# Performance work log

Hardware: AMD Instinct MI355X
Metric: run time of the kernel (lower is better)

Reference implementation:

```python
import jax, jax.numpy as jnp
import numpy as np


def setup_inputs() -> dict:
    key = jax.random.key(0)
    ks = jax.random.split(key, 4)
    B, Tq, Tv, D = 8, 256, 512, 256  # decoder_dim = D = 256
    query = jax.random.normal(ks[0], (B, Tq, D), dtype=jnp.float32)
    value = jax.random.normal(ks[1], (B, Tv, D), dtype=jnp.float32)
    W1 = jax.random.normal(ks[2], (D, D), dtype=jnp.float32) * (1.0 / np.sqrt(D))
    b1 = jnp.zeros((D,), dtype=jnp.float32)
    W2 = jax.random.normal(ks[3], (D, D), dtype=jnp.float32) * (1.0 / np.sqrt(D))
    b2 = jnp.zeros((D,), dtype=jnp.float32)
    return {"query": query, "value": value, "W1": W1, "b1": b1, "W2": W2, "b2": b2}


def reference(query, value, W1, b1, W2, b2):
    # Dense projections: [B,Tq,D], [B,Tv,D]
    q = jnp.einsum('bqd,de->bqe', query, W1) + b1
    v = jnp.einsum('bvd,de->bve', value, W2) + b2
    # Additive (Bahdanau) score: broadcast tanh then reduce over feature dim
    # score: [B,Tq,Tv]  (intermediate [B,Tq,Tv,D] is the fusion target)
    score = jnp.tanh(q[:, :, None, :] + v[:, None, :, :]).sum(axis=-1)
    alignment = jax.nn.softmax(score, axis=-1)  # [B,Tq,Tv]
    context = jnp.einsum('bqv,bvd->bqd', alignment, value)  # [B,Tq,D]
    context = jnp.concatenate([context, query], axis=-1)  # [B,Tq,2D]
    alignment_t = jnp.transpose(alignment, (0, 2, 1))  # [B,Tv,Tq]
    return context, alignment_t
```

## Files before the change

kernel.cpp:

```cpp
#include <hip/hip_runtime.h>

#define B_  8
#define TQ  256
#define TV  512
#define DD  256
#define ALGS 520

__device__ __forceinline__ float fast_exp2(float x) {
#if __has_builtin(__builtin_amdgcn_exp2f)
  return __builtin_amdgcn_exp2f(x);
#else
  return __exp2f(x);
#endif
}
__device__ __forceinline__ float fast_rcp(float x) {
#if __has_builtin(__builtin_amdgcn_rcpf)
  return __builtin_amdgcn_rcpf(x);
#else
  return 1.0f / x;
#endif
}

__global__ __launch_bounds__(256) void proj_fused(
    const float* __restrict__ query, const float* __restrict__ value,
    const float* __restrict__ W1, const float* __restrict__ b1,
    const float* __restrict__ W2, const float* __restrict__ b2,
    float* __restrict__ qp, float* __restrict__ vp, float scale) {
  __shared__ float As[2][32][64];
  __shared__ float Bs[2][32][64];
  const int t  = threadIdx.x;
  const int rt = blockIdx.x;
  const int bn = blockIdx.y << 6;

  const float* A; const float* W; const float* bias; float* out; int row0;
  if (rt < 32) { row0 = rt << 6;        A = query; W = W1; bias = b1; out = qp; }
  else         { row0 = (rt - 32) << 6; A = value; W = W2; bias = b2; out = vp; }

  const int tx = t & 15, ty = t >> 4;
  const int aar = t >> 3, aac = (t & 7) << 2;
  const int bbr = t >> 4, bbc = (t & 15) << 2;

  float4 ra[2], rb[2];
#pragma unroll
  for (int it = 0; it < 2; ++it) {
    ra[it] = *(const float4*)(A + (size_t)(row0 + (it << 5) + aar) * DD + aac);
    rb[it] = *(const float4*)(W + (size_t)((it << 4) + bbr) * DD + bn + bbc);
  }
#pragma unroll
  for (int it = 0; it < 2; ++it) {
    const int m = (it << 5) + aar;
#pragma unroll
    for (int c = 0; c < 4; ++c) {
      const int k = aac + c;
      As[0][k][m ^ (((k >> 2) & 7) << 2)] = (&ra[it].x)[c];
    }
    *(float4*)&Bs[0][(it << 4) + bbr][bbc] = rb[it];
  }
  __syncthreads();

  float acc[4][4] = {{0.f,0.f,0.f,0.f},{0.f,0.f,0.f,0.f},
                     {0.f,0.f,0.f,0.f},{0.f,0.f,0.f,0.f}};
  int p = 0;

  for (int k0 = 0; k0 < 256; k0 += 32) {
    const bool more = (k0 + 32) < 256;
    if (more) {
#pragma unroll
      for (int it = 0; it < 2; ++it) {
        ra[it] = *(const float4*)(A + (size_t)(row0 + (it << 5) + aar) * DD + k0 + 32 + aac);
        rb[it] = *(const float4*)(W + (size_t)(k0 + 32 + (it << 4) + bbr) * DD + bn + bbc);
      }
    }
#pragma unroll
    for (int k = 0; k < 32; ++k) {
      float4 aq = *(const float4*)&As[p][k][(ty << 2) ^ (((k >> 2) & 7) << 2)];
      float4 bq = *(const float4*)&Bs[p][k][tx << 2];
      acc[0][0] = fmaf(aq.x, bq.x, acc[0][0]); acc[0][1] = fmaf(aq.x, bq.y, acc[0][1]);
      acc[0][2] = fmaf(aq.x, bq.z, acc[0][2]); acc[0][3] = fmaf(aq.x, bq.w, acc[0][3]);
      acc[1][0] = fmaf(aq.y, bq.x, acc[1][0]); acc[1][1] = fmaf(aq.y, bq.y, acc[1][1]);
      acc[1][2] = fmaf(aq.y, bq.z, acc[1][2]); acc[1][3] = fmaf(aq.y, bq.w, acc[1][3]);
      acc[2][0] = fmaf(aq.z, bq.x, acc[2][0]); acc[2][1] = fmaf(aq.z, bq.y, acc[2][1]);
      acc[2][2] = fmaf(aq.z, bq.z, acc[2][2]); acc[2][3] = fmaf(aq.z, bq.w, acc[2][3]);
      acc[3][0] = fmaf(aq.w, bq.x, acc[3][0]); acc[3][1] = fmaf(aq.w, bq.y, acc[3][1]);
      acc[3][2] = fmaf(aq.w, bq.z, acc[3][2]); acc[3][3] = fmaf(aq.w, bq.w, acc[3][3]);
    }
    if (more) {
      const int q = p ^ 1;
#pragma unroll
      for (int it = 0; it < 2; ++it) {
        const int m = (it << 5) + aar;
#pragma unroll
        for (int c = 0; c < 4; ++c) {
          const int k = aac + c;
          As[q][k][m ^ (((k >> 2) & 7) << 2)] = (&ra[it].x)[c];
        }
        *(float4*)&Bs[q][(it << 4) + bbr][bbc] = rb[it];
      }
      __syncthreads();
      p = q;
    }
  }

  float4 bvv = *(const float4*)&bias[bn + (tx << 2)];
#pragma unroll
  for (int r = 0; r < 4; ++r) {
    float4 o;
    o.x = fast_exp2(scale * (acc[r][0] + bvv.x));
    o.y = fast_exp2(scale * (acc[r][1] + bvv.y));
    o.z = fast_exp2(scale * (acc[r][2] + bvv.z));
    o.w = fast_exp2(scale * (acc[r][3] + bvv.w));
    *(float4*)(out + (size_t)(row0 + (ty << 2) + r) * DD + bn + (tx << 2)) = o;
  }
}

__global__ __launch_bounds__(512, 4) void attn_kernel(
    const float* __restrict__ qp, const float* __restrict__ vp,
    const float* __restrict__ value, const float* __restrict__ query,
    float* __restrict__ out1, float* __restrict__ out2) {
  __shared__ float qs[4 * 256];
  __shared__ float alg[4 * ALGS];

  const int t    = threadIdx.x;
  const int lane = t & 63;
  const int wv   = t >> 6;
  const int jj   = lane >> 2;
  const int dq   = lane & 3;
  const int bb   = blockIdx.x & 7;
  const int i0   = (blockIdx.x >> 3) << 2;

  const float* vpb = vp + (size_t)bb * TV * DD;
  const float* qb  = qp + (size_t)(bb * TQ + i0) * DD;

  if (t < 256) {
    const int qi = t >> 6, qc = (t & 63) << 2;
    *(float4*)&qs[qi * 256 + qc] = *(const float4*)(qb + (size_t)qi * DD + qc);
  }
  __syncthreads();

  const int jb = (wv << 4) + jj;
  const float* vr0 = vpb + (size_t)jb * DD + (dq << 2);
  const float* vr1 = vr0 + 128 * DD;
  const float* vr2 = vr0 + 256 * DD;
  const float* vr3 = vr0 + 384 * DD;
  const float* qlane = qs + (dq << 2);

  float acc[4][4] = {{0.f,0.f,0.f,0.f},{0.f,0.f,0.f,0.f},
                     {0.f,0.f,0.f,0.f},{0.f,0.f,0.f,0.f}};

#pragma unroll 2
  for (int k = 0; k < 16; ++k) {
    const int doff = k << 4;
    float4 q0 = *(const float4*)(qlane + 0 * 256 + doff);
    float4 q1 = *(const float4*)(qlane + 1 * 256 + doff);
    float4 q2 = *(const float4*)(qlane + 2 * 256 + doff);
    float4 q3 = *(const float4*)(qlane + 3 * 256 + doff);
#pragma unroll
    for (int jg = 0; jg < 4; ++jg) {
      const float* vrp = (jg == 0) ? vr0 : (jg == 1) ? vr1 : (jg == 2) ? vr2 : vr3;
      float4 v4 = *(const float4*)(vrp + doff);
#pragma unroll
      for (int i = 0; i < 4; ++i) {
        const float4 q4 = (i == 0) ? q0 : (i == 1) ? q1 : (i == 2) ? q2 : q3;
        float a = q4.x * v4.x, b = q4.y * v4.y;
        float c = q4.z * v4.z, d = q4.w * v4.w;
        float sab = a + b,  scd = c + d;
        float Q1 = fmaf(a, b, sab + 1.f);
        float Q2 = fmaf(c, d, scd + 1.f);
        float N  = fmaf(scd + 2.f, Q1, (sab + 2.f) * Q2);
        acc[i][jg] = fmaf(N, fast_rcp(Q1 * Q2), acc[i][jg]);
      }
    }
  }

#pragma unroll
  for (int i = 0; i < 4; ++i)
#pragma unroll
    for (int jg = 0; jg < 4; ++jg) {
      acc[i][jg] += __shfl_xor(acc[i][jg], 1, 64);
      acc[i][jg] += __shfl_xor(acc[i][jg], 2, 64);
    }
#pragma unroll
  for (int jg = 0; jg < 4; ++jg) {
    float x = (dq == 0) ? acc[0][jg] : (dq == 1) ? acc[1][jg]
            : (dq == 2) ? acc[2][jg] : acc[3][jg];
    alg[dq * ALGS + (jg << 7) + jb] = x;
  }
  __syncthreads();

  if (wv < 4) {
    float s[8];
#pragma unroll
    for (int c = 0; c < 8; ++c) s[c] = alg[wv * ALGS + (c << 6) + lane];
    float mn = s[0];
#pragma unroll
    for (int c = 1; c < 8; ++c) mn = fminf(mn, s[c]);
#pragma unroll
    for (int m = 1; m < 64; m <<= 1) mn = fminf(mn, __shfl_xor(mn, m, 64));

    const float CC = 2.8853900817779268f;
    float p[8];
    float sum = 0.f;
#pragma unroll
    for (int c = 0; c < 8; ++c) { p[c] = fast_exp2(CC * (mn - s[c])); sum += p[c]; }
#pragma unroll
    for (int m = 1; m < 64; m <<= 1) sum += __shfl_xor(sum, m, 64);
    const float inv = fast_rcp(sum);
#pragma unroll
    for (int c = 0; c < 8; ++c) alg[wv * ALGS + (c << 6) + lane] = p[c] * inv;
  }
  __syncthreads();

  {
    const int j = t;
    float4 av = make_float4(alg[j], alg[ALGS + j], alg[2 * ALGS + j], alg[3 * ALGS + j]);
    *(float4*)(out2 + (size_t)(bb * TV + j) * TQ + i0) = av;
  }

  const int f  = t & 255;
  const int rp = t >> 8;
  float c0 = 0.f, c1 = 0.f;
  const float* vb = value + (size_t)bb * TV * DD;
  const float* a0p = &alg[(2 * rp + 0) * ALGS];
  const float* a1p = &alg[(2 * rp + 1) * ALGS];
#pragma unroll 4
  for (int j = 0; j < TV; j += 4) {
    float v0 = vb[(size_t)(j + 0) * DD + f];
    float v1 = vb[(size_t)(j + 1) * DD + f];
    float v2 = vb[(size_t)(j + 2) * DD + f];
    float v3 = vb[(size_t)(j + 3) * DD + f];
    float4 a0 = *(const float4*)&a0p[j];
    float4 a1 = *(const float4*)&a1p[j];
    c0 += a0.x * v0 + a0.y * v1 + a0.z * v2 + a0.w * v3;
    c1 += a1.x * v0 + a1.y * v1 + a1.z * v2 + a1.w * v3;
  }

  const int r0_ = (rp << 1), r1_ = r0_ + 1;
  const float* qg = query + (size_t)(bb * TQ + i0) * DD;
  float* o = out1 + (size_t)(bb * TQ + i0) * (2 * DD);
  o[r0_ * 512 + f] = c0; o[r0_ * 512 + 256 + f] = qg[r0_ * DD + f];
  o[r1_ * 512 + f] = c1; o[r1_ * 512 + 256 + f] = qg[r1_ * DD + f];
}

extern "C" void kernel_launch(void* const* d_in, const int* in_sizes, int n_in,
                              void* d_out, int out_size, void* d_ws, size_t ws_size,
                              hipStream_t stream) {
  const float* query = (const float*)d_in[0];
  const float* value = (const float*)d_in[1];
  const float* W1    = (const float*)d_in[2];
  const float* b1    = (const float*)d_in[3];
  const float* W2    = (const float*)d_in[4];
  const float* b2    = (const float*)d_in[5];

  float* out1 = (float*)d_out;
  float* out2 = out1 + (size_t)B_ * TQ * 2 * DD;

  float* qp = (float*)d_ws;
  float* vp = qp + (size_t)B_ * TQ * DD;

  const float SC = 2.8853900817779268f;

  proj_fused<<<dim3(96, 4), 256, 0, stream>>>(query, value, W1, b1, W2, b2, qp, vp, SC);
  attn_kernel<<<dim3(B_ * (TQ / 4)), 512, 0, stream>>>(qp, vp, value, query, out1, out2);
}
```

Before: 140.9 us.

## Split context GEMV over Tv across waves with float4 loads and LDS reduction

The context stage is reorganized so that each wave handles a 64-row slice of Tv, and each thread computes a 4-query by 4-feature tile with float4 value loads. Partial sums are then reduced across the 8 waves through a new 32 KB shared-memory buffer. The first four value rows are prefetched before the softmax barrier so their latency overlaps the softmax. The score loop unroll is also raised to 4. The extra LDS raises shared usage per block, which may limit occupancy under launch bounds of (512,4), and it adds a barrier plus a reduction pass.

```diff
diff --git a/kernel.cpp b/kernel.cpp
--- a/kernel.cpp
+++ b/kernel.cpp
@@ -119,6 +119,7 @@
     float* __restrict__ out1, float* __restrict__ out2) {
   __shared__ float qs[4 * 256];
   __shared__ float alg[4 * ALGS];
+  __shared__ float ctxp[8][4][256];
 
   const int t    = threadIdx.x;
   const int lane = t & 63;
@@ -147,7 +148,7 @@
   float acc[4][4] = {{0.f,0.f,0.f,0.f},{0.f,0.f,0.f,0.f},
                      {0.f,0.f,0.f,0.f},{0.f,0.f,0.f,0.f}};
 
-#pragma unroll 2
+#pragma unroll 4
   for (int k = 0; k < 16; ++k) {
     const int doff = k << 4;
     float4 q0 = *(const float4*)(qlane + 0 * 256 + doff);
@@ -185,15 +186,26 @@
             : (dq == 2) ? acc[2][jg] : acc[3][jg];
     alg[dq * ALGS + (jg << 7) + jb] = x;
   }
+
+  const int f4 = (t & 63) << 2;
+  const int s  = t >> 6;
+  const float* vb  = value + (size_t)bb * TV * DD;
+  const float* vsp = vb + (size_t)(s << 6) * DD + f4;
+
+  float4 pv0 = *(const float4*)(vsp + 0 * DD);
+  float4 pv1 = *(const float4*)(vsp + 1 * DD);
+  float4 pv2 = *(const float4*)(vsp + 2 * DD);
+  float4 pv3 = *(const float4*)(vsp + 3 * DD);
+
   __syncthreads();
 
   if (wv < 4) {
-    float s[8];
-#pragma unroll
-    for (int c = 0; c < 8; ++c) s[c] = alg[wv * ALGS + (c << 6) + lane];
-    float mn = s[0];
-#pragma unroll
-    for (int c = 1; c < 8; ++c) mn = fminf(mn, s[c]);
+    float sv[8];
+#pragma unroll
+    for (int c = 0; c < 8; ++c) sv[c] = alg[wv * ALGS + (c << 6) + lane];
+    float mn = sv[0];
+#pragma unroll
+    for (int c = 1; c < 8; ++c) mn = fminf(mn, sv[c]);
 #pragma unroll
     for (int m = 1; m < 64; m <<= 1) mn = fminf(mn, __shfl_xor(mn, m, 64));
 
@@ -201,7 +213,7 @@
     float p[8];
     float sum = 0.f;
 #pragma unroll
-    for (int c = 0; c < 8; ++c) { p[c] = fast_exp2(CC * (mn - s[c])); sum += p[c]; }
+    for (int c = 0; c < 8; ++c) { p[c] = fast_exp2(CC * (mn - sv[c])); sum += p[c]; }
 #pragma unroll
     for (int m = 1; m < 64; m <<= 1) sum += __shfl_xor(sum, m, 64);
     const float inv = fast_rcp(sum);
@@ -216,29 +228,60 @@
     *(float4*)(out2 + (size_t)(bb * TV + j) * TQ + i0) = av;
   }
 
-  const int f  = t & 255;
-  const int rp = t >> 8;
-  float c0 = 0.f, c1 = 0.f;
-  const float* vb = value + (size_t)bb * TV * DD;
-  const float* a0p = &alg[(2 * rp + 0) * ALGS];
-  const float* a1p = &alg[(2 * rp + 1) * ALGS];
+  float c4[4][4] = {{0.f,0.f,0.f,0.f},{0.f,0.f,0.f,0.f},
+                    {0.f,0.f,0.f,0.f},{0.f,0.f,0.f,0.f}};
+  const int jbase = s << 6;
+  {
+#pragma unroll
+    for (int i = 0; i < 4; ++i) {
+      float4 ai = *(const float4*)&alg[i * ALGS + jbase];
+      c4[i][0] = fmaf(ai.x, pv0.x, c4[i][0]); c4[i][1] = fmaf(ai.x, pv0.y, c4[i][1]);
+      c4[i][2] = fmaf(ai.x, pv0.z, c4[i][2]); c4[i][3] = fmaf(ai.x, pv0.w, c4[i][3]);
+      c4[i][0] = fmaf(ai.y, pv1.x, c4[i][0]); c4[i][1] = fmaf(ai.y, pv1.y, c4[i][1]);
+      c4[i][2] = fmaf(ai.y, pv1.z, c4[i][2]); c4[i][3] = fmaf(ai.y, pv1.w, c4[i][3]);
+      c4[i][0] = fmaf(ai.z, pv2.x, c4[i][0]); c4[i][1] = fmaf(ai.z, pv2.y, c4[i][1]);
+      c4[i][2] = fmaf(ai.z, pv2.z, c4[i][2]); c4[i][3] = fmaf(ai.z, pv2.w, c4[i][3]);
+      c4[i][0] = fmaf(ai.w, pv3.x, c4[i][0]); c4[i][1] = fmaf(ai.w, pv3.y, c4[i][1]);
+      c4[i][2] = fmaf(ai.w, pv3.z, c4[i][2]); c4[i][3] = fmaf(ai.w, pv3.w, c4[i][3]);
+    }
+  }
 #pragma unroll 4
-  for (int j = 0; j < TV; j += 4) {
-    float v0 = vb[(size_t)(j + 0) * DD + f];
-    float v1 = vb[(size_t)(j + 1) * DD + f];
-    float v2 = vb[(size_t)(j + 2) * DD + f];
-    float v3 = vb[(size_t)(j + 3) * DD + f];
-    float4 a0 = *(const float4*)&a0p[j];
-    float4 a1 = *(const float4*)&a1p[j];
-    c0 += a0.x * v0 + a0.y * v1 + a0.z * v2 + a0.w * v3;
-    c1 += a1.x * v0 + a1.y * v1 + a1.z * v2 + a1.w * v3;
-  }
-
-  const int r0_ = (rp << 1), r1_ = r0_ + 1;
+  for (int u = 4; u < 64; u += 4) {
+    float4 v0 = *(const float4*)(vsp + (size_t)(u + 0) * DD);
+    float4 v1 = *(const float4*)(vsp + (size_t)(u + 1) * DD);
+    float4 v2 = *(const float4*)(vsp + (size_t)(u + 2) * DD);
+    float4 v3 = *(const float4*)(vsp + (size_t)(u + 3) * DD);
+#pragma unroll
+    for (int i = 0; i < 4; ++i) {
+      float4 ai = *(const float4*)&alg[i * ALGS + jbase + u];
+      c4[i][0] = fmaf(ai.x, v0.x, c4[i][0]); c4[i][1] = fmaf(ai.x, v0.y, c4[i][1]);
+      c4[i][2] = fmaf(ai.x, v0.z, c4[i][2]); c4[i][3] = fmaf(ai.x, v0.w, c4[i][3]);
+      c4[i][0] = fmaf(ai.y, v1.x, c4[i][0]); c4[i][1] = fmaf(ai.y, v1.y, c4[i][1]);
+      c4[i][2] = fmaf(ai.y, v1.z, c4[i][2]); c4[i][3] = fmaf(ai.y, v1.w, c4[i][3]);
+      c4[i][0] = fmaf(ai.z, v2.x, c4[i][0]); c4[i][1] = fmaf(ai.z, v2.y, c4[i][1]);
+      c4[i][2] = fmaf(ai.z, v2.z, c4[i][2]); c4[i][3] = fmaf(ai.z, v2.w, c4[i][3]);
+      c4[i][0] = fmaf(ai.w, v3.x, c4[i][0]); c4[i][1] = fmaf(ai.w, v3.y, c4[i][1]);
+      c4[i][2] = fmaf(ai.w, v3.z, c4[i][2]); c4[i][3] = fmaf(ai.w, v3.w, c4[i][3]);
+    }
+  }
+#pragma unroll
+  for (int i = 0; i < 4; ++i)
+    *(float4*)&ctxp[s][i][f4] = make_float4(c4[i][0], c4[i][1], c4[i][2], c4[i][3]);
+  __syncthreads();
+
   const float* qg = query + (size_t)(bb * TQ + i0) * DD;
   float* o = out1 + (size_t)(bb * TQ + i0) * (2 * DD);
-  o[r0_ * 512 + f] = c0; o[r0_ * 512 + 256 + f] = qg[r0_ * DD + f];
-  o[r1_ * 512 + f] = c1; o[r1_ * 512 + 256 + f] = qg[r1_ * DD + f];
+#pragma unroll
+  for (int it = 0; it < 2; ++it) {
+    const int slot = t + (it << 9);
+    const int ri = slot >> 8;
+    const int ff = slot & 255;
+    float sum = 0.f;
+#pragma unroll
+    for (int ss = 0; ss < 8; ++ss) sum += ctxp[ss][ri][ff];
+    o[ri * 512 + ff] = sum;
+    o[ri * 512 + 256 + ff] = qg[ri * DD + ff];
+  }
 }
 
 extern "C" void kernel_launch(void* const* d_in, const int* in_sizes, int n_in,
```

New measurement: 130.9 us. 7.1% less time.
